# Kernel optimization log

Hardware: AMD Instinct MI355X
Metric: run time of the kernel (lower is better)

The kernel has to match this reference:

```python
import jax, jax.numpy as jnp
import numpy as np

B, C, H, W = 16, 128, 128, 128
HEADS, DH = 4, 32          # hidden_dim = 128
GROUPS = 32                # min(dim // 4, 32)
EPS = 1e-5                 # eqx GroupNorm default


def setup_inputs() -> dict:
    key = jax.random.key(0)
    ks = jax.random.split(key, 8)
    hid = HEADS * DH
    return {
        "x": jax.random.normal(ks[0], (B, C, H, W), jnp.float32),
        "cond": jax.random.normal(ks[1], (B, C, H, W), jnp.float32),
        "gn_scale": jnp.ones((C,), jnp.float32),
        "gn_bias": jnp.zeros((C,), jnp.float32),
        "kv_w": jax.random.normal(ks[2], (2 * hid, C), jnp.float32) * 0.05,
        "kv_b": jax.random.normal(ks[3], (2 * hid,), jnp.float32) * 0.05,
        "q_w": jax.random.normal(ks[4], (hid, C), jnp.float32) * 0.05,
        "q_b": jax.random.normal(ks[5], (hid,), jnp.float32) * 0.05,
        "out_w": jax.random.normal(ks[6], (C, hid), jnp.float32) * 0.05,
        "out_b": jax.random.normal(ks[7], (C,), jnp.float32) * 0.05,
    }


def reference(x, cond, gn_scale, gn_bias, kv_w, kv_b, q_w, q_b, out_w, out_b):
    b, c, h, w = x.shape
    n = h * w
    # --- GroupNorm(32, dim) on x ---
    xg = x.reshape(b, GROUPS, c // GROUPS, h, w)
    mu = xg.mean(axis=(2, 3, 4), keepdims=True)
    var = xg.var(axis=(2, 3, 4), keepdims=True)
    xn = ((xg - mu) * jax.lax.rsqrt(var + EPS)).reshape(b, c, h, w)
    xn = xn * gn_scale[None, :, None, None] + gn_bias[None, :, None, None]
    # --- 1x1 conv projections (channel matmuls) ---
    kv = jnp.einsum('oc,bchw->bohw', kv_w, xn) + kv_b[None, :, None, None]
    q = jnp.einsum('oc,bchw->bohw', q_w, cond) + q_b[None, :, None, None]
    # split: channel layout is (kv, heads, dh)
    kv = kv.reshape(b, 2, HEADS, DH, n)
    k, v = kv[:, 0], kv[:, 1]          # [b, heads, dh, n]
    q = q.reshape(b, HEADS, DH, n)
    # --- linear-time attention: softmax over spatial positions ---
    k = jax.nn.softmax(k, axis=-1)
    context = jnp.einsum('bhdn,bhen->bhde', k, v)   # [b, heads, dh, dh]
    out = jnp.einsum('bhde,bhdn->bhen', context, q)  # [b, heads, dh, n]
    out = out.reshape(b, HEADS * DH, h, w)
    return jnp.einsum('oc,bchw->bohw', out_w, out) + out_b[None, :, None, None]
```

## Files before the change

kernel.cpp:

```cpp
#include <hip/hip_runtime.h>
#include <hip/hip_bf16.h>
#include <cstddef>

#define BATCH 16
#define CC 128
#define NN 16384
#define GROUPS 32
#define EPSV 1e-5f

#define OFF_MU    0
#define OFF_RSTD  512
#define OFF_BEFF  1024
#define OFF_CTX   5120
#define OFF_CB    70656
#define OFF_WH    334848
#define OFF_AH    596992
#define OFF_AL    728064
#define OFF_PART  859136
#define OFF_XT    5184512
#define PART_STRIDE 4224

typedef __attribute__((ext_vector_type(8))) short bf8;
typedef __attribute__((ext_vector_type(4))) float f4;
#define MFMA16(a,b,c) __builtin_amdgcn_mfma_f32_16x16x32_bf16(a,b,c,0,0,0)

__device__ inline unsigned short bf16_rtn(float f) {
    unsigned u = __builtin_bit_cast(unsigned, f);
    unsigned r = (u + 0x7FFFu + ((u >> 16) & 1u)) >> 16;
    return (unsigned short)r;
}
__device__ inline float bf16_f(unsigned short h) {
    unsigned u = ((unsigned)h) << 16;
    return __builtin_bit_cast(float, u);
}
__device__ inline unsigned cvtpk_bf16(float a, float b) {
    unsigned r;
    asm("v_cvt_pk_bf16_f32 %0, %1, %2" : "=v"(r) : "v"(a), "v"(b));
    return r;
}

__global__ __launch_bounds__(256) void k1a_fused(const float* __restrict__ src,
        unsigned short* __restrict__ xt, float* __restrict__ gp) {
    int b = blockIdx.y; int p0 = blockIdx.x * 128; int t = threadIdx.x;
    __shared__ unsigned short lh[128 * 136];
    int p = t & 127, chalf = t >> 7;
    const float* sp = src + (size_t)b * CC * NN + p0 + p;
    #pragma unroll 8
    for (int i = 0; i < 64; ++i) {
        int c = i * 2 + chalf;
        float v = sp[(size_t)c * NN];
        lh[p * 136 + c] = bf16_rtn(v);
    }
    __syncthreads();
    {
        int g = t >> 3, i8 = t & 7;
        float s = 0.f, sq = 0.f;
        for (int pp = i8 * 16; pp < i8 * 16 + 16; ++pp) {
            #pragma unroll
            for (int cc = 0; cc < 4; ++cc) {
                float v = bf16_f(lh[pp * 136 + g * 4 + cc]);
                s += v; sq += v * v;
            }
        }
        __shared__ float rs[256], rq[256];
        rs[t] = s; rq[t] = sq;
        __syncthreads();
        if (t < 32) {
            float a = 0.f, bq = 0.f;
            #pragma unroll
            for (int k = 0; k < 8; ++k) { a += rs[t * 8 + k]; bq += rq[t * 8 + k]; }
            float* d = gp + ((size_t)(b * 128 + blockIdx.x) * 32 + t) * 2;
            d[0] = a; d[1] = bq;
        }
    }
    int pr = t >> 4, c8 = (t & 15) * 8;
    #pragma unroll
    for (int j = 0; j < 8; ++j) {
        int p2 = j * 16 + pr;
        bf8 vh = *(const bf8*)&lh[p2 * 136 + c8];
        *(bf8*)&xt[((size_t)b * NN + p0 + p2) * 128 + c8] = vh;
    }
}

__global__ void k1b_stats(const float* __restrict__ gp, float* __restrict__ wsf) {
    int b = blockIdx.x; int t = threadIdx.x;
    int g = t & 31, sl = t >> 5;
    float s = 0.f, sq = 0.f;
    for (int j = sl; j < 128; j += 8) {
        const float* p = gp + ((size_t)(b * 128 + j) * 32 + g) * 2;
        s += p[0]; sq += p[1];
    }
    __shared__ float rs[256], rq[256];
    rs[t] = s; rq[t] = sq; __syncthreads();
    if (t < 32) {
        #pragma unroll
        for (int k = 1; k < 8; ++k) { s += rs[t + 32 * k]; sq += rq[t + 32 * k]; }
        float mean = s * (1.f / 65536.f);
        float var  = sq * (1.f / 65536.f) - mean * mean;
        wsf[OFF_MU + b * 32 + t]   = mean;
        wsf[OFF_RSTD + b * 32 + t] = rsqrtf(var + EPSV);
    }
}

__global__ void k2_weff(const float* __restrict__ kv_w, const float* __restrict__ kv_b,
                        const float* __restrict__ gn_scale, const float* __restrict__ gn_bias,
                        float* __restrict__ wsf, unsigned short* __restrict__ wh) {
    int b = blockIdx.x, o = threadIdx.x;
    const float* mu = wsf + OFF_MU + b * GROUPS;
    const float* rs = wsf + OFF_RSTD + b * GROUPS;
    float w[128]; float bacc = 0.f;
    #pragma unroll
    for (int c = 0; c < 128; ++c) {
        int g = c >> 2;
        float sc = gn_scale[c] * rs[g];
        float kw = kv_w[o * 128 + c];
        w[c] = kw * sc;
        bacc += kw * (gn_bias[c] - mu[g] * sc);
    }
    wsf[OFF_BEFF + b * 256 + o] = kv_b[o] + bacc;
    int h  = (o & 127) >> 5;
    int ct = ((o >> 4) & 1) + ((o >= 128) ? 2 : 0);
    int i  = o & 15;
    #pragma unroll
    for (int ks = 0; ks < 4; ++ks)
      #pragma unroll
      for (int eq = 0; eq < 4; ++eq) {
        bf8 pk;
        #pragma unroll
        for (int e = 0; e < 8; ++e) pk[e] = (short)bf16_rtn(w[ks*32 + eq*8 + e]);
        int lane = i + 16 * eq;
        size_t fo = ((((size_t)b * 4 + h) * 4 + ct) * 4 + ks) * 512 + (size_t)lane * 8;
        *(bf8*)&wh[fo] = pk;
      }
}

__global__ __launch_bounds__(256) void k3_attn(
    const unsigned short* __restrict__ xt,
    const unsigned short* __restrict__ wh, const float* __restrict__ wsf,
    float* __restrict__ part)
{
    int b = blockIdx.y, chunk = blockIdx.x;
    int t = threadIdx.x, h = t >> 6, l = t & 63;
    int l15 = l & 15, lq = l >> 4;

    __shared__ unsigned short lds[4][2][32 * 64];

    bf8 W[4][4];
    #pragma unroll
    for (int ct = 0; ct < 4; ++ct)
      #pragma unroll
      for (int ks = 0; ks < 4; ++ks)
        W[ct][ks] = ((const bf8*)wh)[((((size_t)b*4 + h)*4 + ct)*4 + ks)*64 + l];

    float bk[4];
    #pragma unroll
    for (int ct = 0; ct < 4; ++ct) {
        int o = (ct < 2) ? (32*h + 16*ct + l15) : (128 + 32*h + 16*(ct-2) + l15);
        bk[ct] = wsf[OFF_BEFF + b * 256 + o];
    }

    bf8 ones;
    #pragma unroll
    for (int j = 0; j < 8; ++j) ones[j] = (short)0x3F80;

    f4 ctx[2][2]; f4 zac[2];
    #pragma unroll
    for (int i = 0; i < 2; ++i) {
        zac[i] = (f4){0,0,0,0};
        #pragma unroll
        for (int j = 0; j < 2; ++j) ctx[i][j] = (f4){0,0,0,0};
    }

    int pbase = chunk * 256;
    for (int tile = 0; tile < 4; ++tile) {
        int tp = pbase + tile * 64;
        #pragma unroll
        for (int pt = 0; pt < 4; ++pt) {
            f4 a4[4];
            #pragma unroll
            for (int ct = 0; ct < 4; ++ct) a4[ct] = (f4){0,0,0,0};
            size_t rowoff = ((size_t)b * NN + tp + pt*16 + l15) * 128 + lq * 8;
            #pragma unroll
            for (int ks = 0; ks < 4; ++ks) {
                bf8 ah = *(const bf8*)(xt + rowoff + ks*32);
                #pragma unroll
                for (int ct = 0; ct < 4; ++ct)
                    a4[ct] = MFMA16(ah, W[ct][ks], a4[ct]);
            }
            int p = pt * 16 + lq * 4;
            #pragma unroll
            for (int ct = 0; ct < 4; ++ct) {
                int row = (ct & 1) * 16 + l15;
                int sel = ct >> 1;
                unsigned short pk[4];
                #pragma unroll
                for (int j = 0; j < 4; ++j) {
                    float v = a4[ct][j] + bk[ct];
                    if (sel == 0) v = __expf(v);
                    pk[j] = bf16_rtn(v);
                }
                unsigned byte = ((unsigned)(row * 128 + p * 2)) ^ (((unsigned)(row & 7)) << 4);
                unsigned lo32 = (unsigned)pk[0] | ((unsigned)pk[1] << 16);
                unsigned hi32 = (unsigned)pk[2] | ((unsigned)pk[3] << 16);
                *(uint2*)((char*)&lds[h][sel][0] + byte) = make_uint2(lo32, hi32);
            }
        }
        #pragma unroll
        for (int ks2 = 0; ks2 < 2; ++ks2) {
            int p8 = ks2 * 32 + lq * 8;
            bf8 ek[2], vv[2];
            #pragma unroll
            for (int dt = 0; dt < 2; ++dt) {
                int row = dt * 16 + l15;
                unsigned byte = ((unsigned)(row * 128 + p8 * 2)) ^ (((unsigned)(row & 7)) << 4);
                ek[dt] = *(const bf8*)((char*)&lds[h][0][0] + byte);
                vv[dt] = *(const bf8*)((char*)&lds[h][1][0] + byte);
            }
            #pragma unroll
            for (int dt = 0; dt < 2; ++dt) {
                #pragma unroll
                for (int et = 0; et < 2; ++et)
                    ctx[dt][et] = MFMA16(ek[dt], vv[et], ctx[dt][et]);
                zac[dt] = MFMA16(ek[dt], ones, zac[dt]);
            }
        }
    }
    float* pb = part + (size_t)(b * 64 + chunk) * PART_STRIDE;
    #pragma unroll
    for (int dt = 0; dt < 2; ++dt) {
        #pragma unroll
        for (int et = 0; et < 2; ++et)
            #pragma unroll
            for (int j = 0; j < 4; ++j) {
                int d = 32*h + dt*16 + lq*4 + j;
                int e = et*16 + l15;
                pb[d * 32 + e] = ctx[dt][et][j];
            }
        if (l15 == 0)
            #pragma unroll
            for (int j = 0; j < 4; ++j)
                pb[4096 + 32*h + dt*16 + lq*4 + j] = zac[dt][j];
    }
}

__global__ __launch_bounds__(256) void k4_reduce(const float* __restrict__ part,
                                                 float* __restrict__ wsf, int nbpb) {
    int q = blockIdx.x, b = blockIdx.y;
    int tid = threadIdx.x;
    int hdl = tid >> 3;
    int hd = q * 32 + hdl;
    int e0 = (tid & 7) * 4;
    float s[4] = {0.f, 0.f, 0.f, 0.f};
    float z = 0.f;
    for (int i = 0; i < nbpb; ++i) {
        const float* pb = part + (size_t)(b * nbpb + i) * PART_STRIDE;
        float4 v = *(const float4*)&pb[hd * 32 + e0];
        s[0] += v.x; s[1] += v.y; s[2] += v.z; s[3] += v.w;
        if ((tid & 7) == 0) z += pb[4096 + hd];
    }
    __shared__ float zs[32];
    if ((tid & 7) == 0) zs[hdl] = z;
    __syncthreads();
    float zi = 1.f / zs[hdl];
    float* cg = wsf + OFF_CTX + (size_t)b * 4096;
    #pragma unroll
    for (int j = 0; j < 4; ++j) cg[hd * 32 + e0 + j] = s[j] * zi;
}

__global__ __launch_bounds__(256) void k5_buildA(const float* __restrict__ out_w,
                          const float* __restrict__ q_w,
                          const float* __restrict__ q_b, const float* __restrict__ out_b,
                          float* __restrict__ wsf,
                          unsigned short* __restrict__ ahp, unsigned short* __restrict__ alp) {
    int b = blockIdx.y;
    int oh = blockIdx.x * 16;
    int tid = threadIdx.x;
    __shared__ float ctx_p[128 * 33];
    __shared__ float T_s[16 * 132];
    {
        const float* src = wsf + OFF_CTX + (size_t)b * 4096;
        for (int i = tid; i < 4096; i += 256)
            ctx_p[(i >> 5) * 33 + (i & 31)] = src[i];
    }
    __syncthreads();
    int ol = tid >> 4;
    int o = oh + ol;
    int jb = tid & 15;
    int j0 = jb * 8;
    int h = j0 >> 5;
    {
        float ow[32];
        #pragma unroll
        for (int e4 = 0; e4 < 8; ++e4) {
            float4 v = *(const float4*)&out_w[o * 128 + h * 32 + e4 * 4];
            ow[e4*4+0]=v.x; ow[e4*4+1]=v.y; ow[e4*4+2]=v.z; ow[e4*4+3]=v.w;
        }
        #pragma unroll
        for (int dd = 0; dd < 8; ++dd) {
            int r = h * 32 + (j0 & 31) + dd;
            const float* cp = &ctx_p[r * 33];
            float a0 = 0.f, a1 = 0.f, a2 = 0.f, a3 = 0.f;
            #pragma unroll
            for (int e = 0; e < 32; e += 4) {
                a0 += ow[e+0] * cp[e+0];
                a1 += ow[e+1] * cp[e+1];
                a2 += ow[e+2] * cp[e+2];
                a3 += ow[e+3] * cp[e+3];
            }
            T_s[ol * 132 + j0 + dd] = (a0 + a1) + (a2 + a3);
        }
    }
    __syncthreads();
    {
        int ci0 = jb * 8;
        float a[8];
        #pragma unroll
        for (int i = 0; i < 8; ++i) a[i] = 0.f;
        for (int j = 0; j < 128; ++j) {
            float tv = T_s[ol * 132 + j];
            float4 v0 = *(const float4*)&q_w[j * 128 + ci0];
            float4 v1 = *(const float4*)&q_w[j * 128 + ci0 + 4];
            a[0] += tv*v0.x; a[1] += tv*v0.y; a[2] += tv*v0.z; a[3] += tv*v0.w;
            a[4] += tv*v1.x; a[5] += tv*v1.y; a[6] += tv*v1.z; a[7] += tv*v1.w;
        }
        int ks = ci0 >> 5;
        int eq = (ci0 >> 3) & 3;
        int lane = (o & 15) + 16 * eq;
        bf8 ph, pl;
        #pragma unroll
        for (int e = 0; e < 8; ++e) {
            unsigned short hh = bf16_rtn(a[e]);
            ph[e] = (short)hh;
            pl[e] = (short)bf16_rtn(a[e] - bf16_f(hh));
        }
        size_t fo = ((((size_t)b * 8 + (o >> 4)) * 4 + ks) * 64 + lane) * 8;
        *(bf8*)&ahp[fo] = ph;
        *(bf8*)&alp[fo] = pl;
        if (jb == 0) {
            float cb = 0.f;
            for (int j = 0; j < 128; ++j) cb += T_s[ol * 132 + j] * q_b[j];
            wsf[OFF_CB + b * 128 + o] = cb + out_b[o];
        }
    }
}

__global__ __launch_bounds__(256) void k6_mfma(
    const float* __restrict__ cond,
    const unsigned short* __restrict__ ahp, const unsigned short* __restrict__ alp,
    const float* __restrict__ wsf, float* __restrict__ y)
{
    int b = blockIdx.y, chunk = blockIdx.x;
    int t = threadIdx.x, w = t >> 6, l = t & 63, l15 = l & 15, lq = l >> 4;

    __shared__ __align__(16) unsigned short bfr[4][4][2][512];

    bf8 Ah[2][4], Al[2][4];
    #pragma unroll
    for (int r = 0; r < 2; ++r)
      #pragma unroll
      for (int ks = 0; ks < 4; ++ks) {
        size_t idx = (((size_t)b * 8 + (2*w + r)) * 4 + ks) * 64 + l;
        Ah[r][ks] = ((const bf8*)ahp)[idx];
        Al[r][ks] = ((const bf8*)alp)[idx];
      }
    float cbl[2][4];
    #pragma unroll
    for (int r = 0; r < 2; ++r)
      #pragma unroll
      for (int j = 0; j < 4; ++j)
        cbl[r][j] = wsf[OFF_CB + b*128 + (2*w + r)*16 + lq*4 + j];

    int pbase = chunk * 128;
    for (int tile = 0; tile < 2; ++tile) {
        int tp = pbase + tile * 64;
        if (tile > 0) __syncthreads();
        {
            const float* cp = cond + (size_t)b * 128 * NN + tp + w*16 + l15;
            #pragma unroll
            for (int ks = 0; ks < 4; ++ks) {
                float v[8];
                #pragma unroll
                for (int j = 0; j < 8; ++j)
                    v[j] = cp[(size_t)(ks*32 + lq*8 + j) * NN];
                union { unsigned u[4]; bf8 s; } uh, ul;
                #pragma unroll
                for (int q = 0; q < 4; ++q) {
                    unsigned hp = cvtpk_bf16(v[2*q], v[2*q+1]);
                    uh.u[q] = hp;
                    float f0 = __builtin_bit_cast(float, hp << 16);
                    float f1 = __builtin_bit_cast(float, hp & 0xFFFF0000u);
                    ul.u[q] = cvtpk_bf16(v[2*q] - f0, v[2*q+1] - f1);
                }
                *(bf8*)&bfr[w][ks][0][l * 8] = uh.s;
                *(bf8*)&bfr[w][ks][1][l * 8] = ul.s;
            }
        }
        __syncthreads();
        f4 acc[2][4];
        #pragma unroll
        for (int r = 0; r < 2; ++r)
          #pragma unroll
          for (int pt = 0; pt < 4; ++pt) acc[r][pt] = (f4){0,0,0,0};
        #pragma unroll
        for (int pt = 0; pt < 4; ++pt) {
            #pragma unroll
            for (int ks = 0; ks < 4; ++ks) {
                bf8 bh = *(const bf8*)&bfr[pt][ks][0][l * 8];
                bf8 bl = *(const bf8*)&bfr[pt][ks][1][l * 8];
                #pragma unroll
                for (int r = 0; r < 2; ++r) {
                    acc[r][pt] = MFMA16(Ah[r][ks], bh, acc[r][pt]);
                    acc[r][pt] = MFMA16(Al[r][ks], bh, acc[r][pt]);
                    acc[r][pt] = MFMA16(Ah[r][ks], bl, acc[r][pt]);
                }
            }
        }
        #pragma unroll
        for (int r = 0; r < 2; ++r)
          #pragma unroll
          for (int pt = 0; pt < 4; ++pt)
            #pragma unroll
            for (int j = 0; j < 4; ++j) {
                int o = (2*w + r)*16 + lq*4 + j;
                int p = tp + pt*16 + l15;
                y[((size_t)b*128 + o)*NN + p] = acc[r][pt][j] + cbl[r][j];
            }
    }
}

extern "C" void kernel_launch(void* const* d_in, const int* in_sizes, int n_in,
                              void* d_out, int out_size, void* d_ws, size_t ws_size,
                              hipStream_t stream) {
    const float* x        = (const float*)d_in[0];
    const float* cond     = (const float*)d_in[1];
    const float* gn_scale = (const float*)d_in[2];
    const float* gn_bias  = (const float*)d_in[3];
    const float* kv_w     = (const float*)d_in[4];
    const float* kv_b     = (const float*)d_in[5];
    const float* q_w      = (const float*)d_in[6];
    const float* q_b      = (const float*)d_in[7];
    const float* out_w    = (const float*)d_in[8];
    const float* out_b    = (const float*)d_in[9];
    float* y   = (float*)d_out;
    float* wsf = (float*)d_ws;

    unsigned short* WH = (unsigned short*)(wsf + OFF_WH);
    unsigned short* AH = (unsigned short*)(wsf + OFF_AH);
    unsigned short* AL = (unsigned short*)(wsf + OFF_AL);
    float* part = wsf + OFF_PART;

    bool big = ws_size >= (size_t)(OFF_XT + 16777216) * sizeof(float);

    unsigned short* XT;
    if (big) {
        XT = (unsigned short*)(wsf + OFF_XT);
    } else {
        XT = (unsigned short*)y;
    }

    k1a_fused<<<dim3(128, BATCH), 256, 0, stream>>>(x, XT, part);
    k1b_stats<<<BATCH, 256, 0, stream>>>(part, wsf);
    k2_weff<<<16, 256, 0, stream>>>(kv_w, kv_b, gn_scale, gn_bias, wsf, WH);
    k3_attn<<<dim3(64, BATCH), 256, 0, stream>>>(XT, WH, wsf, part);
    k4_reduce<<<dim3(4, BATCH), 256, 0, stream>>>(part, wsf, 64);
    k5_buildA<<<dim3(8, BATCH), 256, 0, stream>>>(out_w, q_w, q_b, out_b, wsf, AH, AL);
    k6_mfma<<<dim3(128, BATCH), 256, 0, stream>>>(cond, AH, AL, wsf, y);
}
```

Measured before the change: 206.8 us.

## Parallelize weight-fold kernel across blocks and widen k6 pixel tiles

The GroupNorm-folded KV weight kernel goes from 16 blocks, each thread handling a full 128-wide row in registers, to 8x16 blocks that stage 32 weight rows in shared memory and split each row's work across 8 threads with a shared-memory reduction for the bias. The final MFMA output kernel now has each block process 4 pixel tiles instead of 2, halving its grid. This amortizes the per-block loads of A fragments and bias, at the cost of fewer blocks in flight.

After: 212.6 us. 1.03x slower.

```diff
diff --git a/kernel.cpp b/kernel.cpp
--- a/kernel.cpp
+++ b/kernel.cpp
@@ -102,36 +102,63 @@
     }
 }
 
-__global__ void k2_weff(const float* __restrict__ kv_w, const float* __restrict__ kv_b,
+__global__ __launch_bounds__(256) void k2_weff(const float* __restrict__ kv_w,
+                        const float* __restrict__ kv_b,
                         const float* __restrict__ gn_scale, const float* __restrict__ gn_bias,
                         float* __restrict__ wsf, unsigned short* __restrict__ wh) {
-    int b = blockIdx.x, o = threadIdx.x;
-    const float* mu = wsf + OFF_MU + b * GROUPS;
-    const float* rs = wsf + OFF_RSTD + b * GROUPS;
-    float w[128]; float bacc = 0.f;
-    #pragma unroll
-    for (int c = 0; c < 128; ++c) {
-        int g = c >> 2;
-        float sc = gn_scale[c] * rs[g];
-        float kw = kv_w[o * 128 + c];
-        w[c] = kw * sc;
-        bacc += kw * (gn_bias[c] - mu[g] * sc);
-    }
-    wsf[OFF_BEFF + b * 256 + o] = kv_b[o] + bacc;
+    int b = blockIdx.y;
+    int o0 = blockIdx.x * 32;
+    int t = threadIdx.x;
+    __shared__ float wrow[32 * 128];
+    __shared__ float scl[128], sbm[128];
+    __shared__ float bred[32][8];
+    {
+        const float4* src = (const float4*)(kv_w + (size_t)o0 * 128);
+        float4* dst = (float4*)wrow;
+        #pragma unroll
+        for (int i = 0; i < 4; ++i) dst[i * 256 + t] = src[i * 256 + t];
+        if (t < 128) {
+            int g = t >> 2;
+            float r = wsf[OFF_RSTD + b * 32 + g];
+            float m = wsf[OFF_MU + b * 32 + g];
+            float sc = gn_scale[t] * r;
+            scl[t] = sc;
+            sbm[t] = gn_bias[t] - m * sc;
+        }
+    }
+    __syncthreads();
+    int ol = t >> 3;
+    int o  = o0 + ol;
+    int q  = t & 7;
+    {
+        float bacc = 0.f;
+        const float* wr = &wrow[ol * 128 + q * 16];
+        #pragma unroll
+        for (int c = 0; c < 16; ++c) bacc += wr[c] * sbm[q * 16 + c];
+        bred[ol][q] = bacc;
+    }
     int h  = (o & 127) >> 5;
     int ct = ((o >> 4) & 1) + ((o >= 128) ? 2 : 0);
-    int i  = o & 15;
-    #pragma unroll
-    for (int ks = 0; ks < 4; ++ks)
-      #pragma unroll
-      for (int eq = 0; eq < 4; ++eq) {
+    #pragma unroll
+    for (int f2 = 0; f2 < 2; ++f2) {
+        int f = 2 * q + f2;
+        int ks = f >> 2, eq = f & 3;
+        int c0 = ks * 32 + eq * 8;
         bf8 pk;
         #pragma unroll
-        for (int e = 0; e < 8; ++e) pk[e] = (short)bf16_rtn(w[ks*32 + eq*8 + e]);
-        int lane = i + 16 * eq;
+        for (int e = 0; e < 8; ++e)
+            pk[e] = (short)bf16_rtn(wrow[ol * 128 + c0 + e] * scl[c0 + e]);
+        int lane = (o & 15) + 16 * eq;
         size_t fo = ((((size_t)b * 4 + h) * 4 + ct) * 4 + ks) * 512 + (size_t)lane * 8;
         *(bf8*)&wh[fo] = pk;
-      }
+    }
+    __syncthreads();
+    if (q == 0) {
+        float bacc = 0.f;
+        #pragma unroll
+        for (int k = 0; k < 8; ++k) bacc += bred[ol][k];
+        wsf[OFF_BEFF + b * 256 + o] = kv_b[o] + bacc;
+    }
 }
 
 __global__ __launch_bounds__(256) void k3_attn(
@@ -370,8 +397,8 @@
       for (int j = 0; j < 4; ++j)
         cbl[r][j] = wsf[OFF_CB + b*128 + (2*w + r)*16 + lq*4 + j];
 
-    int pbase = chunk * 128;
-    for (int tile = 0; tile < 2; ++tile) {
+    int pbase = chunk * 256;
+    for (int tile = 0; tile < 4; ++tile) {
         int tp = pbase + tile * 64;
         if (tile > 0) __syncthreads();
         {
@@ -460,9 +487,9 @@
 
     k1a_fused<<<dim3(128, BATCH), 256, 0, stream>>>(x, XT, part);
     k1b_stats<<<BATCH, 256, 0, stream>>>(part, wsf);
-    k2_weff<<<16, 256, 0, stream>>>(kv_w, kv_b, gn_scale, gn_bias, wsf, WH);
+    k2_weff<<<dim3(8, BATCH), 256, 0, stream>>>(kv_w, kv_b, gn_scale, gn_bias, wsf, WH);
     k3_attn<<<dim3(64, BATCH), 256, 0, stream>>>(XT, WH, wsf, part);
     k4_reduce<<<dim3(4, BATCH), 256, 0, stream>>>(part, wsf, 64);
     k5_buildA<<<dim3(8, BATCH), 256, 0, stream>>>(out_w, q_w, q_b, out_b, wsf, AH, AL);
-    k6_mfma<<<dim3(128, BATCH), 256, 0, stream>>>(cond, AH, AL, wsf, y);
-}
+    k6_mfma<<<dim3(64, BATCH), 256, 0, stream>>>(cond, AH, AL, wsf, y);
+}
```
